# Optimization experiments

Measured on AMD Instinct MI355X. Metric: run time of the kernel, lower is better.

## Reference

```python
import jax, jax.numpy as jnp
import numpy as np

B, S, D = 2, 2048, 2048
H, HD = 16, 128
WINDOW = 512
ROPE_BASE = 10000.0


def setup_inputs() -> dict:
    key = jax.random.key(0)
    k1, k2, k3 = jax.random.split(key, 3)
    x = jax.random.normal(k1, (B, S, D), dtype=jnp.float32)
    w_qkv = jax.random.normal(k2, (3 * D, D), dtype=jnp.float32) * (D ** -0.5)
    w_out = jax.random.normal(k3, (D, D), dtype=jnp.float32) * (D ** -0.5)
    return {"x": x, "w_qkv": w_qkv, "w_out": w_out}


def _rope_cos_sin(seq_len, head_dim, base, dtype):
    inv_freq = 1.0 / (base ** (jnp.arange(0, head_dim, 2, dtype=jnp.float32) / head_dim))
    pos = jnp.arange(seq_len, dtype=jnp.float32)
    freqs = pos[:, None] * inv_freq[None, :]            # (S, HD/2)
    emb = jnp.concatenate([freqs, freqs], axis=-1)       # (S, HD)
    return jnp.cos(emb).astype(dtype), jnp.sin(emb).astype(dtype)


def _rotate_half(x):
    x1, x2 = jnp.split(x, 2, axis=-1)
    return jnp.concatenate([-x2, x1], axis=-1)


def reference(x, w_qkv, w_out):
    Bx, Sx, Dx = x.shape
    # fused QKV projection (torch Linear: x @ W^T)
    qkv = jnp.einsum('bsd,ed->bse', x, w_qkv)
    q, k, v = jnp.split(qkv, 3, axis=-1)
    q = q.reshape(Bx, Sx, H, HD).transpose(0, 2, 1, 3)   # (B,H,S,HD)
    k = k.reshape(Bx, Sx, H, HD).transpose(0, 2, 1, 3)
    v = v.reshape(Bx, Sx, H, HD).transpose(0, 2, 1, 3)
    # RoPE with implicit position_ids = arange(S)
    cos, sin = _rope_cos_sin(Sx, HD, ROPE_BASE, x.dtype)  # (S, HD)
    q = q * cos[None, None] + _rotate_half(q) * sin[None, None]
    k = k * cos[None, None] + _rotate_half(k) * sin[None, None]
    # sliding-window attention: attend iff 0 <= i - j < WINDOW
    scale = 1.0 / jnp.sqrt(jnp.array(HD, dtype=x.dtype))
    scores = jnp.einsum('bhqd,bhkd->bhqk', q, k) * scale
    i = jnp.arange(Sx)[:, None]
    j = jnp.arange(Sx)[None, :]
    diff = i - j
    valid = (diff >= 0) & (diff < WINDOW)                # (S, S)
    scores = jnp.where(valid[None, None], scores, jnp.finfo(scores.dtype).min)
    attn = jax.nn.softmax(scores, axis=-1)
    out = jnp.einsum('bhqk,bhkd->bhqd', attn, v)
    out = out.transpose(0, 2, 1, 3).reshape(Bx, Sx, Dx)
    return jnp.einsum('bsd,ed->bse', out, w_out)
```

## Files before the change

kernel.cpp:

```cpp
#include <hip/hip_runtime.h>

#define S_LEN 2048
#define DIM 2048
#define NH 16
#define HD 128
#define WIN 512
#define QKVD (3 * DIM)

typedef unsigned short u16;
typedef __bf16 bf16x8 __attribute__((ext_vector_type(8)));
typedef float f32x4 __attribute__((ext_vector_type(4)));

__device__ __forceinline__ u16 f2bf(float f) {
  unsigned u = __builtin_bit_cast(unsigned, f);
  u += 0x7FFFu + ((u >> 16) & 1u);
  return (u16)(u >> 16);
}
__device__ __forceinline__ float bf2f(u16 b) {
  return __builtin_bit_cast(float, (unsigned)b << 16);
}
__device__ __forceinline__ void async16(const void* g, void* l) {
  __builtin_amdgcn_global_load_lds((__attribute__((address_space(1))) void*)g,
                                   (__attribute__((address_space(3))) void*)l,
                                   16, 0, 0);
}

__global__ __launch_bounds__(256) void cvt_kernel(const float* __restrict__ in,
                                                  u16* __restrict__ out, int n) {
  int i = (blockIdx.x * 256 + threadIdx.x) * 4;
  if (i < n) {
    float4 v = *(const float4*)(in + i);
    ushort4 o;
    o.x = f2bf(v.x); o.y = f2bf(v.y); o.z = f2bf(v.z); o.w = f2bf(v.w);
    *(ushort4*)(out + i) = o;
  }
}

__global__ __launch_bounds__(256) void rope_tab_kernel(float* __restrict__ cosT,
                                                       float* __restrict__ sinT) {
  int idx = blockIdx.x * 256 + threadIdx.x;
  int s = idx >> 6, j = idx & 63;
  double freq = exp((double)j * -0.14391156831212787);
  double a = (double)s * freq;
  cosT[idx] = (float)cos(a);
  sinT[idx] = (float)sin(a);
}

template <typename TO>
__global__ __launch_bounds__(256, 2) void gemm_bt(const u16* __restrict__ A,
                                                  const u16* __restrict__ B,
                                                  TO* __restrict__ C,
                                                  int M, int N, int K) {
  __shared__ __align__(16) u16 As[128 * 64];
  __shared__ __align__(16) u16 Bs[128 * 64];
  const int tiles_n = N >> 7;
  const int m0 = (blockIdx.x / tiles_n) << 7;
  const int n0 = (blockIdx.x % tiles_n) << 7;
  const int t = threadIdx.x;
  const int l = t & 63, w = t >> 6;
  const int wr = w >> 1, wc = w & 1;
  const int l16 = l & 15, lg = l >> 4;
  f32x4 acc[4][4] = {};
  for (int k0 = 0; k0 < K; k0 += 64) {
    __syncthreads();
#pragma unroll
    for (int i = 0; i < 4; ++i) {
      int c = t + (i << 8);
      int r = c >> 3, cc = c & 7;
      async16(A + (size_t)(m0 + r) * K + k0 + cc * 8, (char*)As + c * 16);
    }
#pragma unroll
    for (int i = 0; i < 4; ++i) {
      int c = t + (i << 8);
      int r = c >> 3, cc = c & 7;
      async16(B + (size_t)(n0 + r) * K + k0 + cc * 8, (char*)Bs + c * 16);
    }
    __syncthreads();
#pragma unroll
    for (int ks = 0; ks < 2; ++ks) {
      bf16x8 af[4], bfv[4];
#pragma unroll
      for (int m = 0; m < 4; ++m)
        af[m] = *(const bf16x8*)(As + (wr * 64 + m * 16 + l16) * 64 + ks * 32 + lg * 8);
#pragma unroll
      for (int n = 0; n < 4; ++n)
        bfv[n] = *(const bf16x8*)(Bs + (wc * 64 + n * 16 + l16) * 64 + ks * 32 + lg * 8);
#pragma unroll
      for (int m = 0; m < 4; ++m)
#pragma unroll
        for (int n = 0; n < 4; ++n)
          acc[m][n] = __builtin_amdgcn_mfma_f32_16x16x32_bf16(af[m], bfv[n], acc[m][n], 0, 0, 0);
    }
  }
  const int rb = m0 + wr * 64 + lg * 4;
  const int cb = n0 + wc * 64 + l16;
#pragma unroll
  for (int m = 0; m < 4; ++m)
#pragma unroll
    for (int n = 0; n < 4; ++n)
#pragma unroll
      for (int r = 0; r < 4; ++r) {
        float v = acc[m][n][r];
        size_t idx = (size_t)(rb + m * 16 + r) * N + cb + n * 16;
        if constexpr (sizeof(TO) == 2) C[idx] = f2bf(v);
        else C[idx] = v;
      }
}

__global__ __launch_bounds__(256) void rope_kernel(u16* __restrict__ qkv,
                                                   const float* __restrict__ cosT,
                                                   const float* __restrict__ sinT) {
  const int row = blockIdx.x;
  const int s = row & (S_LEN - 1);
  const int t = threadIdx.x;
  u16* base = qkv + (size_t)row * QKVD;
#pragma unroll
  for (int j = 0; j < 4; ++j) {
    const int pi = t + j * 256;
    const int h = pi >> 6, d = pi & 63;
    const float c = cosT[(s << 6) + d];
    const float sn = sinT[(s << 6) + d];
    u16* q = base + h * HD;
    float q1 = bf2f(q[d]), q2 = bf2f(q[d + 64]);
    q[d] = f2bf(q1 * c - q2 * sn);
    q[d + 64] = f2bf(q2 * c + q1 * sn);
    u16* k = base + DIM + h * HD;
    float k1 = bf2f(k[d]), k2 = bf2f(k[d + 64]);
    k[d] = f2bf(k1 * c - k2 * sn);
    k[d + 64] = f2bf(k2 * c + k1 * sn);
  }
}

__global__ __launch_bounds__(512, 4) void attn_kernel(const u16* __restrict__ qkv,
                                                      u16* __restrict__ attnO) {
  const int bid = blockIdx.x;
  const int qt = bid & 15;
  const int bh = bid >> 4;
  const int q0 = qt << 7;
  const int b = bh >> 4, h = bh & 15;
  const u16* Qp = qkv + (size_t)b * S_LEN * QKVD + h * HD;
  const u16* Kp = Qp + DIM;
  const u16* Vp = Qp + 2 * DIM;
  __shared__ __align__(16) char Ks[64 * 256];
  __shared__ __align__(16) u16 Vt[128][72];
  __shared__ __align__(16) __bf16 Ps[8][16 * 72];
  const int t = threadIdx.x;
  const int w = t >> 6, l = t & 63;
  const int l16 = l & 15, lg = l >> 4;
  const int q0w = q0 + w * 16;
  bf16x8 qf[4];
  {
    const u16* qrow = Qp + (size_t)(q0w + l16) * QKVD;
#pragma unroll
    for (int ks = 0; ks < 4; ++ks) qf[ks] = *(const bf16x8*)(qrow + ks * 32 + lg * 8);
  }
  f32x4 oacc[8] = {};
  float mrow[4], lrow[4];
#pragma unroll
  for (int r = 0; r < 4; ++r) { mrow[r] = -1e30f; lrow[r] = 0.f; }
  const int lo = max(0, (q0 - (WIN - 1)) >> 6);
  const int hi = (q0 + 127) >> 6;
  const int lo_w = max(0, (q0w - (WIN - 1)) >> 6);
  const int hi_w = (q0w + 15) >> 6;
  for (int kt = lo; kt <= hi; ++kt) {
    const int kv0 = kt << 6;
    __syncthreads();
#pragma unroll
    for (int i = 0; i < 2; ++i) {
      int c = t + (i << 9);
      int row = c >> 4, ch = c & 15;
      int sch = ch ^ (row & 7);
      async16(Kp + (size_t)(kv0 + row) * QKVD + sch * 8, Ks + c * 16);
    }
    {
      const int dc = t & 15, pp = t >> 4;
      const int kv = pp * 2, d0 = dc * 8;
      const uint4 va = *(const uint4*)(Vp + (size_t)(kv0 + kv) * QKVD + d0);
      const uint4 vb = *(const uint4*)(Vp + (size_t)(kv0 + kv + 1) * QKVD + d0);
      unsigned av[4] = {va.x, va.y, va.z, va.w};
      unsigned bv[4] = {vb.x, vb.y, vb.z, vb.w};
#pragma unroll
      for (int j = 0; j < 4; ++j) {
        *(unsigned*)&Vt[d0 + j * 2][kv] = (av[j] & 0xffffu) | (bv[j] << 16);
        *(unsigned*)&Vt[d0 + j * 2 + 1][kv] = (av[j] >> 16) | (bv[j] & 0xffff0000u);
      }
    }
    __syncthreads();
    if (kt < lo_w || kt > hi_w) continue;
    f32x4 sc[4];
#pragma unroll
    for (int c4 = 0; c4 < 4; ++c4) {
      f32x4 sa = {};
#pragma unroll
      for (int ks = 0; ks < 4; ++ks) {
        const int krow = c4 * 16 + l16;
        const int ch = (ks * 4 + lg) ^ (krow & 7);
        bf16x8 kf = *(const bf16x8*)(Ks + krow * 256 + ch * 16);
        sa = __builtin_amdgcn_mfma_f32_16x16x32_bf16(qf[ks], kf, sa, 0, 0, 0);
      }
      sc[c4] = sa;
    }
    const float scale = 0.08838834764831843f;
    const int qi_base = q0w + lg * 4;
    float pm[4];
#pragma unroll
    for (int r = 0; r < 4; ++r) pm[r] = -1e30f;
#pragma unroll
    for (int c4 = 0; c4 < 4; ++c4) {
      const int kj = kv0 + c4 * 16 + l16;
#pragma unroll
      for (int r = 0; r < 4; ++r) {
        const int diff = qi_base + r - kj;
        float v = sc[c4][r] * scale;
        v = (diff >= 0 && diff < WIN) ? v : -1e30f;
        sc[c4][r] = v;
        pm[r] = fmaxf(pm[r], v);
      }
    }
#pragma unroll
    for (int off = 1; off < 16; off <<= 1)
#pragma unroll
      for (int r = 0; r < 4; ++r) pm[r] = fmaxf(pm[r], __shfl_xor(pm[r], off));
    float scl[4];
#pragma unroll
    for (int r = 0; r < 4; ++r) {
      float mn = fmaxf(mrow[r], pm[r]);
      scl[r] = expf(mrow[r] - mn);
      mrow[r] = mn;
    }
    __bf16* pp2 = Ps[w];
    float ps[4] = {0.f, 0.f, 0.f, 0.f};
#pragma unroll
    for (int c4 = 0; c4 < 4; ++c4)
#pragma unroll
      for (int r = 0; r < 4; ++r) {
        float p = expf(sc[c4][r] - mrow[r]);
        ps[r] += p;
        pp2[(lg * 4 + r) * 72 + c4 * 16 + l16] = (__bf16)p;
      }
#pragma unroll
    for (int off = 1; off < 16; off <<= 1)
#pragma unroll
      for (int r = 0; r < 4; ++r) ps[r] += __shfl_xor(ps[r], off);
#pragma unroll
    for (int r = 0; r < 4; ++r) lrow[r] = lrow[r] * scl[r] + ps[r];
#pragma unroll
    for (int dt = 0; dt < 8; ++dt) {
      f32x4 o = oacc[dt];
#pragma unroll
      for (int r = 0; r < 4; ++r) o[r] *= scl[r];
      oacc[dt] = o;
    }
    asm volatile("" ::: "memory");
#pragma unroll
    for (int ks = 0; ks < 2; ++ks) {
      bf16x8 pf = *(const bf16x8*)(pp2 + l16 * 72 + ks * 32 + lg * 8);
#pragma unroll
      for (int dt = 0; dt < 8; ++dt) {
        bf16x8 vf = *(const bf16x8*)(&Vt[dt * 16 + l16][ks * 32 + lg * 8]);
        oacc[dt] = __builtin_amdgcn_mfma_f32_16x16x32_bf16(pf, vf, oacc[dt], 0, 0, 0);
      }
    }
  }
  const int qi = q0w + lg * 4;
  u16* orow = attnO + ((size_t)(b * S_LEN + qi) * DIM) + h * HD;
#pragma unroll
  for (int r = 0; r < 4; ++r) {
    float inv = 1.f / lrow[r];
#pragma unroll
    for (int dt = 0; dt < 8; ++dt)
      orow[(size_t)r * DIM + dt * 16 + l16] = f2bf(oacc[dt][r] * inv);
  }
}

extern "C" void kernel_launch(void* const* d_in, const int* in_sizes, int n_in,
                              void* d_out, int out_size, void* d_ws, size_t ws_size,
                              hipStream_t stream) {
  const float* x = (const float*)d_in[0];
  const float* w_qkv = (const float*)d_in[1];
  const float* w_out = (const float*)d_in[2];
  float* out = (float*)d_out;

  char* ws = (char*)d_ws;
  size_t off = 0;
  auto alloc = [&](size_t bytes) {
    void* p = ws + off;
    off = (off + bytes + 255) & ~(size_t)255;
    return p;
  };
  const size_t rows = 2ull * S_LEN;
  u16* wqkvb = (u16*)alloc(3ull * DIM * DIM * 2);
  u16* woutb = (u16*)alloc((size_t)DIM * DIM * 2);
  u16* xb    = (u16*)alloc(rows * DIM * 2);
  u16* qkvb  = (u16*)alloc(rows * 3 * DIM * 2);
  float* cosT = (float*)alloc((size_t)S_LEN * 64 * 4);
  float* sinT = (float*)alloc((size_t)S_LEN * 64 * 4);

  cvt_kernel<<<(3 * DIM * DIM) / 1024, 256, 0, stream>>>(w_qkv, wqkvb, 3 * DIM * DIM);
  cvt_kernel<<<(DIM * DIM) / 1024, 256, 0, stream>>>(w_out, woutb, DIM * DIM);
  cvt_kernel<<<(int)(rows * DIM / 1024), 256, 0, stream>>>(x, xb, (int)(rows * DIM));
  rope_tab_kernel<<<(S_LEN * 64) / 256, 256, 0, stream>>>(cosT, sinT);
  gemm_bt<u16><<<(int)(rows / 128) * (QKVD / 128), 256, 0, stream>>>(
      xb, wqkvb, qkvb, (int)rows, QKVD, DIM);
  rope_kernel<<<(int)rows, 256, 0, stream>>>(qkvb, cosT, sinT);
  u16* attnb = wqkvb;
  attn_kernel<<<2 * NH * (S_LEN / 128), 512, 0, stream>>>(qkvb, attnb);
  gemm_bt<float><<<(int)(rows / 128) * (DIM / 128), 256, 0, stream>>>(
      attnb, woutb, out, (int)rows, DIM, DIM);
}
```

Before: 275.3 us.

## Add 256x256-tile 8-wave pipelined GEMM for QKV projection

```diff
diff --git a/kernel.cpp b/kernel.cpp
--- a/kernel.cpp
+++ b/kernel.cpp
@@ -24,6 +24,7 @@
                                    (__attribute__((address_space(3))) void*)l,
                                    16, 0, 0);
 }
+#define WAITV6 asm volatile("s_waitcnt vmcnt(6)" ::: "memory")
 
 __global__ __launch_bounds__(256) void cvt_kernel(const float* __restrict__ in,
                                                   u16* __restrict__ out, int n) {
@@ -44,6 +45,126 @@
   double a = (double)s * freq;
   cosT[idx] = (float)cos(a);
   sinT[idx] = (float)sin(a);
+}
+
+__global__ __launch_bounds__(512, 2) void gemm8(const u16* __restrict__ A,
+                                                const u16* __restrict__ B,
+                                                u16* __restrict__ C,
+                                                int M, int N, int K) {
+  constexpr int ABY = 256 * 128;
+  __shared__ __align__(16) char Al[2 * ABY];
+  __shared__ __align__(16) char Bl[2 * ABY];
+
+  const int tiles_n = N >> 8;
+  const int nwg = gridDim.x;
+  const int wg = ((int)blockIdx.x & 7) * (nwg >> 3) + ((int)blockIdx.x >> 3);
+  const int m0 = (wg / tiles_n) << 8;
+  const int n0 = (wg % tiles_n) << 8;
+  const int t = threadIdx.x;
+  const int l = t & 63, w = t >> 6;
+  const int wr = w >> 2, wc = w & 3;
+  const int l16 = l & 15, lg = l >> 4;
+  const u16* Asrc = A + (size_t)m0 * K;
+  const u16* Bsrc = B + (size_t)n0 * K;
+
+  auto stA = [&](int kcol, int half, int b) {
+#pragma unroll
+    for (int j = 0; j < 2; ++j) {
+      int c = t + j * 512;
+      int rih = c >> 3, ch = c & 7;
+      int row = (rih & 63) | ((rih >> 6) << 7) | (half << 6);
+      async16(Asrc + (size_t)row * K + kcol + ((ch ^ (row & 7)) << 3),
+              Al + b * ABY + row * 128 + ch * 16);
+    }
+  };
+  auto stB = [&](int kcol, int half, int b) {
+#pragma unroll
+    for (int j = 0; j < 2; ++j) {
+      int c = t + j * 512;
+      int rih = c >> 3, ch = c & 7;
+      int row = (rih & 31) | ((rih >> 5) << 6) | (half << 5);
+      async16(Bsrc + (size_t)row * K + kcol + ((ch ^ (row & 7)) << 3),
+              Bl + b * ABY + row * 128 + ch * 16);
+    }
+  };
+
+  f32x4 acc[8][4] = {};
+  bf16x8 af[4][2];
+  bf16x8 bfr[2][2][2];
+
+  auto rdA = [&](int b, int mh) {
+#pragma unroll
+    for (int m = 0; m < 4; ++m)
+#pragma unroll
+      for (int ks = 0; ks < 2; ++ks) {
+        int row = wr * 128 + mh * 64 + m * 16 + l16;
+        int ch = ks * 4 + lg;
+        af[m][ks] = *(const bf16x8*)(Al + b * ABY + row * 128 + ((ch ^ (row & 7)) << 4));
+      }
+  };
+  auto rdB = [&](int b, int nh) {
+#pragma unroll
+    for (int n = 0; n < 2; ++n)
+#pragma unroll
+      for (int ks = 0; ks < 2; ++ks) {
+        int row = wc * 64 + nh * 32 + n * 16 + l16;
+        int ch = ks * 4 + lg;
+        bfr[nh][n][ks] = *(const bf16x8*)(Bl + b * ABY + row * 128 + ((ch ^ (row & 7)) << 4));
+      }
+  };
+  auto mm = [&](int mh, int nh) {
+#pragma unroll
+    for (int m = 0; m < 4; ++m)
+#pragma unroll
+      for (int n = 0; n < 2; ++n)
+#pragma unroll
+        for (int ks = 0; ks < 2; ++ks)
+          acc[mh * 4 + m][nh * 2 + n] = __builtin_amdgcn_mfma_f32_16x16x32_bf16(
+              af[m][ks], bfr[nh][n][ks], acc[mh * 4 + m][nh * 2 + n], 0, 0, 0);
+  };
+
+  const int NT = K >> 6;
+  stA(0, 0, 0); stB(0, 0, 0); stB(0, 1, 0); stA(0, 1, 0); stA(64, 0, 1);
+  WAITV6;
+  __builtin_amdgcn_s_barrier();
+
+  for (int kt = 0; kt < NT; ++kt) {
+    const int b = kt & 1, nb = b ^ 1;
+    const int k1 = ((kt + 1 < NT) ? kt + 1 : kt) << 6;
+    const int k2 = ((kt + 2 < NT) ? kt + 2 : kt) << 6;
+    rdA(b, 0); rdB(b, 0);
+    stB(k1, 0, nb);
+    __builtin_amdgcn_s_barrier();
+    __builtin_amdgcn_s_setprio(1); mm(0, 0); __builtin_amdgcn_s_setprio(0);
+    WAITV6;
+    __builtin_amdgcn_s_barrier();
+    rdB(b, 1);
+    stB(k1, 1, nb);
+    __builtin_amdgcn_s_barrier();
+    __builtin_amdgcn_s_setprio(1); mm(0, 1); __builtin_amdgcn_s_setprio(0);
+    WAITV6;
+    __builtin_amdgcn_s_barrier();
+    rdA(b, 1);
+    stA(k1, 1, nb);
+    __builtin_amdgcn_s_barrier();
+    __builtin_amdgcn_s_setprio(1); mm(1, 0); __builtin_amdgcn_s_setprio(0);
+    __builtin_amdgcn_s_barrier();
+    stA(k2, 0, b);
+    __builtin_amdgcn_s_barrier();
+    __builtin_amdgcn_s_setprio(1); mm(1, 1); __builtin_amdgcn_s_setprio(0);
+    WAITV6;
+    __builtin_amdgcn_s_barrier();
+  }
+
+  const int rb = m0 + wr * 128 + lg * 4;
+  const int cb = n0 + wc * 64 + l16;
+#pragma unroll
+  for (int mi = 0; mi < 8; ++mi)
+#pragma unroll
+    for (int ni = 0; ni < 4; ++ni)
+#pragma unroll
+      for (int r = 0; r < 4; ++r)
+        C[(size_t)(rb + mi * 16 + r) * N + cb + ni * 16] = f2bf(acc[mi][ni][r]);
 }
 
 template <typename TO>
@@ -300,7 +421,7 @@
   cvt_kernel<<<(DIM * DIM) / 1024, 256, 0, stream>>>(w_out, woutb, DIM * DIM);
   cvt_kernel<<<(int)(rows * DIM / 1024), 256, 0, stream>>>(x, xb, (int)(rows * DIM));
   rope_tab_kernel<<<(S_LEN * 64) / 256, 256, 0, stream>>>(cosT, sinT);
-  gemm_bt<u16><<<(int)(rows / 128) * (QKVD / 128), 256, 0, stream>>>(
+  gemm8<<<(int)(rows / 256) * (QKVD / 256), 512, 0, stream>>>(
       xb, wqkvb, qkvb, (int)rows, QKVD, DIM);
   rope_kernel<<<(int)rows, 256, 0, stream>>>(qkvb, cosT, sinT);
   u16* attnb = wqkvb;
```

Result: no change. 272.8 us (-0.9%).
